# Kernel tuning notes

Measured on AMD Instinct MI355X. Metric: run time of the kernel, lower is better.

The kernel has to match this reference:

```python
import jax, jax.numpy as jnp
import numpy as np

E = 1024  # embed_dim
H = 16    # num_heads
D = E // H  # head_dim
B, S = 2, 2048

def _xavier(key, shape):
    fan_in, fan_out = shape[1], shape[0]
    limit = float(np.sqrt(6.0 / (fan_in + fan_out)))
    return jax.random.uniform(key, shape, jnp.float32, -limit, limit)

def setup_inputs() -> dict:
    key = jax.random.key(0)
    ks = jax.random.split(key, 7)
    return {
        "query": jax.random.normal(ks[0], (B, S, E), jnp.float32),
        "key": jax.random.normal(ks[1], (B, S, E), jnp.float32),
        "value": jax.random.normal(ks[2], (B, S, E), jnp.float32),
        "Wq": _xavier(ks[3], (E, E)), "bq": jnp.zeros((E,), jnp.float32),
        "Wk": _xavier(ks[4], (E, E)), "bk": jnp.zeros((E,), jnp.float32),
        "Wv": _xavier(ks[5], (E, E)), "bv": jnp.zeros((E,), jnp.float32),
        "Wo": _xavier(ks[6], (E, E)), "bo": jnp.zeros((E,), jnp.float32),
    }

def reference(query, key, value, Wq, bq, Wk, bk, Wv, bv, Wo, bo):
    b, s, e = query.shape
    # nn.Linear: x @ W^T + b
    Q = (query @ Wq.T + bq).reshape(b, s, H, D).transpose(0, 2, 1, 3)  # [b,h,s,d]
    K = (key @ Wk.T + bk).reshape(b, s, H, D).transpose(0, 2, 1, 3)
    V = (value @ Wv.T + bv).reshape(b, s, H, D).transpose(0, 2, 1, 3)
    scale = D ** -0.5
    scores = jnp.einsum('bhqd,bhkd->bhqk', Q, K) * scale  # [b,h,s,s]
    attn = jax.nn.softmax(scores, axis=-1)  # dropout=0.0 -> identity
    out = jnp.einsum('bhqk,bhkd->bhqd', attn, V)
    out = out.transpose(0, 2, 1, 3).reshape(b, s, e)
    return out @ Wo.T + bo
```

## Files before the change

kernel.cpp:

```cpp
#include <hip/hip_runtime.h>
#include <stdint.h>

#define E_DIM 1024
#define N_HEADS 16
#define HEAD_D 64
#define BATCH 2
#define SEQ 2048
#define M_ROWS (BATCH*SEQ)

typedef __attribute__((ext_vector_type(8))) short short8;
typedef __attribute__((ext_vector_type(4))) short short4_t;
typedef __attribute__((ext_vector_type(4))) float f32x4;
typedef __attribute__((ext_vector_type(4))) int i32x4;
typedef __attribute__((ext_vector_type(2))) int i32x2;

__device__ __forceinline__ unsigned short f2bf(float f) {
  uint32_t u = __float_as_uint(f);
  u += 0x7FFFu + ((u >> 16) & 1u);
  return (unsigned short)(u >> 16);
}

__device__ __forceinline__ void gload_lds16(const void* g, void* l) {
  __builtin_amdgcn_global_load_lds(
      (const __attribute__((address_space(1))) uint32_t*)(uintptr_t)g,
      (__attribute__((address_space(3))) uint32_t*)(uint32_t)(uintptr_t)l,
      16, 0, 0);
}

__device__ __forceinline__ int cvtpk(float lo, float hi) {
  int r;
  asm("v_cvt_pk_bf16_f32 %0, %1, %2" : "=v"(r) : "v"(lo), "v"(hi));
  return r;
}

__device__ __forceinline__ void cvt_body(const float* __restrict__ src,
                                         unsigned short* __restrict__ dst, int i) {
  f32x4 a = ((const f32x4*)src)[2*i];
  f32x4 b = ((const f32x4*)src)[2*i + 1];
  union { unsigned short us[8]; i32x4 v; } o;
  o.us[0] = f2bf(a[0]); o.us[1] = f2bf(a[1]);
  o.us[2] = f2bf(a[2]); o.us[3] = f2bf(a[3]);
  o.us[4] = f2bf(b[0]); o.us[5] = f2bf(b[1]);
  o.us[6] = f2bf(b[2]); o.us[7] = f2bf(b[3]);
  ((i32x4*)dst)[i] = o.v;
}

__global__ void cvt_all(const float* __restrict__ x0, const float* __restrict__ x1,
                        const float* __restrict__ x2,
                        const float* __restrict__ w0, const float* __restrict__ w1,
                        const float* __restrict__ w2, const float* __restrict__ w3,
                        unsigned short* __restrict__ dx0, unsigned short* __restrict__ dx1,
                        unsigned short* __restrict__ dx2,
                        unsigned short* __restrict__ dw0, unsigned short* __restrict__ dw1,
                        unsigned short* __restrict__ dw2, unsigned short* __restrict__ dw3) {
  const int i = blockIdx.x * blockDim.x + threadIdx.x;
  constexpr int NX8 = M_ROWS * E_DIM / 8;
  constexpr int NW8 = E_DIM * E_DIM / 8;
  if (i < 3 * NX8) {
    const int r = i >> 19, off = i & (NX8 - 1);
    const float* s = (r == 0) ? x0 : (r == 1) ? x1 : x2;
    unsigned short* d = (r == 0) ? dx0 : (r == 1) ? dx1 : dx2;
    cvt_body(s, d, off);
  } else {
    const int j = i - 3 * NX8;
    const int r = j >> 17, off = j & (NW8 - 1);
    const float* s = (r == 0) ? w0 : (r == 1) ? w1 : (r == 2) ? w2 : w3;
    unsigned short* d = (r == 0) ? dw0 : (r == 1) ? dw1 : (r == 2) ? dw2 : dw3;
    cvt_body(s, d, off);
  }
}

__device__ __forceinline__ void gemm_body_rt8(const unsigned short* __restrict__ A,
                                              const unsigned short* __restrict__ Bm,
                                              const float* __restrict__ bias,
                                              unsigned short* __restrict__ Cout,
                                              float scale, int bx, int by,
                                              int Nstr, bool brow) {
  constexpr int BM = 128, BN = 128, BK = 64, K = E_DIM;
  __shared__ __attribute__((aligned(16))) unsigned short Al[2][BM*BK];
  __shared__ __attribute__((aligned(16))) unsigned short Bl[2][BN*BK];
  const int tid  = threadIdx.x;
  const int lane = tid & 63, w = tid >> 6;
  const int wm = w >> 2, wn = w & 3;
  const int l15 = lane & 15, l4 = lane >> 4, l7 = lane & 7;
  const int m0 = by * BM, n0 = bx * BN;
  const int jr = lane >> 3, jc = lane & 7;
  const int kcg = jc ^ jr;

#define GSTAGE(KT, BUF)                                                        \
  do {                                                                         \
    _Pragma("unroll")                                                          \
    for (int t = 0; t < 2; ++t) {                                              \
      int ia = w*2 + t;                                                        \
      const char* src = (const char*)A +                                       \
          ((size_t)(m0 + ia*8 + jr)*K + (KT))*2 + (kcg << 4);                  \
      gload_lds16(src, (char*)Al[BUF] + ia*1024);                              \
    }                                                                          \
    _Pragma("unroll")                                                          \
    for (int t = 0; t < 2; ++t) {                                              \
      int ib = w*2 + t;                                                        \
      const char* src = (const char*)Bm +                                      \
          ((size_t)(n0 + ib*8 + jr)*K + (KT))*2 + (kcg << 4);                  \
      gload_lds16(src, (char*)Bl[BUF] + ib*1024);                              \
    }                                                                          \
  } while (0)

  f32x4 zero = {0.f, 0.f, 0.f, 0.f};
  f32x4 acc[4][2];
  for (int i = 0; i < 4; ++i) for (int j = 0; j < 2; ++j) acc[i][j] = zero;

  GSTAGE(0, 0);
  __syncthreads();

  int cur = 0;
  const int NKT = K / BK;
  for (int kt = 0; kt < NKT; ++kt) {
    if (kt + 1 < NKT) GSTAGE((kt + 1) * BK, cur ^ 1);

#pragma unroll
    for (int ks = 0; ks < 2; ++ks) {
      const int sw = ((ks*4 + l4) ^ l7) << 4;
      short8 af[4], bf[2];
#pragma unroll
      for (int mf = 0; mf < 4; ++mf)
        af[mf] = *(const short8*)((const char*)Al[cur] + (wm*64 + mf*16 + l15)*128 + sw);
#pragma unroll
      for (int nf = 0; nf < 2; ++nf)
        bf[nf] = *(const short8*)((const char*)Bl[cur] + (wn*32 + nf*16 + l15)*128 + sw);
      __builtin_amdgcn_s_setprio(1);
#pragma unroll
      for (int mf = 0; mf < 4; ++mf)
#pragma unroll
        for (int nf = 0; nf < 2; ++nf)
          acc[mf][nf] = __builtin_amdgcn_mfma_f32_16x16x32_bf16(
              af[mf], bf[nf], acc[mf][nf], 0, 0, 0);
      __builtin_amdgcn_s_setprio(0);
    }

    __syncthreads();
    cur ^= 1;
  }
#undef GSTAGE

#pragma unroll
  for (int nf = 0; nf < 2; ++nf) {
    const int col = n0 + wn*32 + nf*16 + l15;
    const float bcol = brow ? 0.f : bias[col];
#pragma unroll
    for (int mf = 0; mf < 4; ++mf) {
      const int rowb = m0 + wm*64 + mf*16 + l4*4;
#pragma unroll
      for (int r = 0; r < 4; ++r) {
        const float bv = brow ? bias[rowb + r] : bcol;
        float v = (acc[mf][nf][r] + bv) * scale;
        Cout[(size_t)(rowb + r)*Nstr + col] = f2bf(v);
      }
    }
  }
}

__global__ __launch_bounds__(512, 4)
void gemm_qkv(const unsigned short* __restrict__ Xq, const unsigned short* __restrict__ Xk,
              const unsigned short* __restrict__ Xv,
              const unsigned short* __restrict__ Wq, const unsigned short* __restrict__ Wk,
              const unsigned short* __restrict__ Wv,
              const float* __restrict__ bq, const float* __restrict__ bk,
              const float* __restrict__ bv,
              unsigned short* __restrict__ Qb, unsigned short* __restrict__ Kb,
              unsigned short* __restrict__ Vt, float scale0) {
  const int z = blockIdx.z;
  const int idx = blockIdx.x;
  if (z == 2) {
    gemm_body_rt8(Wv, Xv, bv, Vt, 1.0f, idx & 31, idx >> 5, M_ROWS, true);
  } else {
    const unsigned short* A  = (z == 0) ? Xq : Xk;
    const unsigned short* Bm = (z == 0) ? Wq : Wk;
    const float* bias        = (z == 0) ? bq : bk;
    unsigned short* C        = (z == 0) ? Qb : Kb;
    const float scale        = (z == 0) ? scale0 : 1.0f;
    gemm_body_rt8(A, Bm, bias, C, scale, idx & 7, idx >> 3, E_DIM, false);
  }
}

__global__ __launch_bounds__(256, 2)
void gemm_o(const unsigned short* __restrict__ A, const unsigned short* __restrict__ Bm,
            const float* __restrict__ bias, float* __restrict__ Cout) {
  constexpr int BM = 128, BN = 64, BK = 64, K = E_DIM, N = E_DIM;
  __shared__ __attribute__((aligned(16))) unsigned short Al[2][BM*BK];
  __shared__ __attribute__((aligned(16))) unsigned short Bl[2][BN*BK];
  const int tid  = threadIdx.x;
  const int lane = tid & 63, w = tid >> 6;
  const int wm = w >> 1, wn = w & 1;
  const int l15 = lane & 15, l4 = lane >> 4, l7 = lane & 7;
  const int m0 = blockIdx.y * BM, n0 = blockIdx.x * BN;
  const int jr = lane >> 3, jc = lane & 7;
  const int kcg = jc ^ jr;

#define GSTAGE(KT, BUF)                                                        \
  do {                                                                         \
    _Pragma("unroll")                                                          \
    for (int t = 0; t < 4; ++t) {                                              \
      int ia = w*4 + t;                                                        \
      const char* src = (const char*)A +                                       \
          ((size_t)(m0 + ia*8 + jr)*K + (KT))*2 + (kcg << 4);                  \
      gload_lds16(src, (char*)Al[BUF] + ia*1024);                              \
    }                                                                          \
    _Pragma("unroll")                                                          \
    for (int t = 0; t < 2; ++t) {                                              \
      int ib = w*2 + t;                                                        \
      const char* src = (const char*)Bm +                                      \
          ((size_t)(n0 + ib*8 + jr)*K + (KT))*2 + (kcg << 4);                  \
      gload_lds16(src, (char*)Bl[BUF] + ib*1024);                              \
    }                                                                          \
  } while (0)

  f32x4 zero = {0.f, 0.f, 0.f, 0.f};
  f32x4 acc[4][2];
  for (int i = 0; i < 4; ++i) for (int j = 0; j < 2; ++j) acc[i][j] = zero;

  GSTAGE(0, 0);
  __syncthreads();

  int cur = 0;
  const int NKT = K / BK;
  for (int kt = 0; kt < NKT; ++kt) {
    if (kt + 1 < NKT) GSTAGE((kt + 1) * BK, cur ^ 1);
#pragma unroll
    for (int ks = 0; ks < 2; ++ks) {
      const int sw = ((ks*4 + l4) ^ l7) << 4;
      short8 af[4], bf[2];
#pragma unroll
      for (int mf = 0; mf < 4; ++mf)
        af[mf] = *(const short8*)((const char*)Al[cur] + (wm*64 + mf*16 + l15)*128 + sw);
#pragma unroll
      for (int nf = 0; nf < 2; ++nf)
        bf[nf] = *(const short8*)((const char*)Bl[cur] + (wn*32 + nf*16 + l15)*128 + sw);
      __builtin_amdgcn_s_setprio(1);
#pragma unroll
      for (int mf = 0; mf < 4; ++mf)
#pragma unroll
        for (int nf = 0; nf < 2; ++nf)
          acc[mf][nf] = __builtin_amdgcn_mfma_f32_16x16x32_bf16(
              af[mf], bf[nf], acc[mf][nf], 0, 0, 0);
      __builtin_amdgcn_s_setprio(0);
    }
    __syncthreads();
    cur ^= 1;
  }
#undef GSTAGE

#pragma unroll
  for (int nf = 0; nf < 2; ++nf) {
    const int col = n0 + wn*32 + nf*16 + l15;
    const float bv = bias[col];
#pragma unroll
    for (int mf = 0; mf < 4; ++mf) {
      const int rowb = m0 + wm*64 + mf*16 + l4*4;
#pragma unroll
      for (int r = 0; r < 4; ++r)
        Cout[(size_t)(rowb + r)*N + col] = acc[mf][nf][r] + bv;
    }
  }
}

__global__ __launch_bounds__(512, 2)
void attn_fwd7(const unsigned short* __restrict__ Q,
               const unsigned short* __restrict__ Kg,
               const unsigned short* __restrict__ Vt_g,
               unsigned short* __restrict__ O) {
  __shared__ __attribute__((aligned(16))) unsigned short Kl[2][4096];
  __shared__ __attribute__((aligned(16))) unsigned short Vl[2][4096];
  __shared__ __attribute__((aligned(16))) unsigned short Pl[8][2][1024];

  const int tid = threadIdx.x;
  const int l = tid & 63, w = tid >> 6;
  const int l15 = l & 15, l4 = l >> 4, l7 = l & 7;

  const int id = blockIdx.x;
  const int bh = (id & 7) * 4 + ((id >> 3) & 3);
  const int qt = id >> 5;
  const int b = bh >> 4, h = bh & 15;
  const size_t bS = (size_t)b * SEQ;
  const int qw = qt * 256 + w * 32;

  short8 qf[2][2];
#pragma unroll
  for (int g = 0; g < 2; ++g) {
    const char* qp = (const char*)Q + ((bS + qw + g*16 + l15) * E_DIM + h * 64) * 2;
    qf[g][0] = *(const short8*)(qp + l4 * 16);
    qf[g][1] = *(const short8*)(qp + 64 + l4 * 16);
  }

  f32x4 zero = {0.f, 0.f, 0.f, 0.f};
  f32x4 oacc[2][4];
#pragma unroll
  for (int g = 0; g < 2; ++g)
#pragma unroll
    for (int i = 0; i < 4; ++i) oacc[g][i] = zero;
  float mrow[2] = {-1e30f, -1e30f}, lrow[2] = {0.f, 0.f};

  const int krow = l >> 3;
  const int kcg  = (l & 7) ^ krow;
  const char* vt_base = (const char*)Vt_g +
      ((size_t)(h * 64 + 8 * w + krow) * M_ROWS + bS) * 2 + (kcg << 4);

#define KSTAGE(KT, BUF)                                                        \
  gload_lds16((const char*)Kg +                                                \
                  ((bS + (size_t)(KT)*64 + 8*w + krow) * E_DIM + h*64 + kcg*8)*2, \
              (char*)Kl[BUF] + w * 1024)

#define VSTAGE(KT, BUF)                                                        \
  gload_lds16(vt_base + (size_t)(KT) * 128, (char*)Vl[BUF] + w * 1024)

  KSTAGE(0, 0);
  VSTAGE(0, 0);
  __syncthreads();

  int cur = 0;
  constexpr int NT = SEQ / 64;
  for (int kt = 0; kt < NT; ++kt) {
    const bool more = (kt + 1 < NT);
    if (more) {
      KSTAGE(kt + 1, cur ^ 1);
      VSTAGE(kt + 1, cur ^ 1);
    }

    short8 kf[8];
    {
      const char* kb = (const char*)Kl[cur];
#pragma unroll
      for (int nf = 0; nf < 4; ++nf) {
        const char* rowb = kb + (nf * 16 + l15) * 128;
        kf[nf*2]     = *(const short8*)(rowb + ((l4 ^ l7) << 4));
        kf[nf*2 + 1] = *(const short8*)(rowb + (((4 + l4) ^ l7) << 4));
      }
    }

    short8 pf[2][2];
#pragma unroll
    for (int g = 0; g < 2; ++g) {
      f32x4 s[4];
      __builtin_amdgcn_s_setprio(1);
#pragma unroll
      for (int nf = 0; nf < 4; ++nf) {
        f32x4 z = zero;
        z = __builtin_amdgcn_mfma_f32_16x16x32_bf16(kf[nf*2],     qf[g][0], z, 0, 0, 0);
        z = __builtin_amdgcn_mfma_f32_16x16x32_bf16(kf[nf*2 + 1], qf[g][1], z, 0, 0, 0);
        s[nf] = z;
      }
      __builtin_amdgcn_s_setprio(0);

      float mx = s[0][0];
#pragma unroll
      for (int nf = 0; nf < 4; ++nf)
#pragma unroll
        for (int r = 0; r < 4; ++r) mx = fmaxf(mx, s[nf][r]);
      mx = fmaxf(mx, __shfl_xor(mx, 16));
      mx = fmaxf(mx, __shfl_xor(mx, 32));
      const float mnew = fmaxf(mrow[g], mx);
      const float fac = __builtin_amdgcn_exp2f(mrow[g] - mnew);
      mrow[g] = mnew;

      float pv[4][4];
      float rs = 0.f;
#pragma unroll
      for (int nf = 0; nf < 4; ++nf)
#pragma unroll
        for (int r = 0; r < 4; ++r) {
          float p = __builtin_amdgcn_exp2f(s[nf][r] - mnew);
          pv[nf][r] = p;
          rs += p;
        }
      rs += __shfl_xor(rs, 16);
      rs += __shfl_xor(rs, 32);
      lrow[g] = lrow[g] * fac + rs;

#pragma unroll
      for (int df = 0; df < 4; ++df)
#pragma unroll
        for (int r = 0; r < 4; ++r) oacc[g][df][r] *= fac;

      char* pw = (char*)&Pl[w][g][0];
#pragma unroll
      for (int nf = 0; nf < 4; ++nf) {
        const int c = nf * 2 + (l4 >> 1);
        i32x2 pk;
        pk.x = cvtpk(pv[nf][0], pv[nf][1]);
        pk.y = cvtpk(pv[nf][2], pv[nf][3]);
        *(i32x2*)(pw + l15 * 128 + ((c ^ l7) << 4) + ((l4 & 1) << 3)) = pk;
      }
      pf[g][0] = *(const short8*)(pw + l15 * 128 + ((l4 ^ l7) << 4));
      pf[g][1] = *(const short8*)(pw + l15 * 128 + (((4 + l4) ^ l7) << 4));
    }

    {
      const char* vbuf = (const char*)Vl[cur];
      __builtin_amdgcn_s_setprio(1);
#pragma unroll
      for (int df = 0; df < 4; ++df) {
        const char* rowb = vbuf + (df * 16 + l15) * 128;
        short8 v0 = *(const short8*)(rowb + ((l4 ^ l7) << 4));
        short8 v1 = *(const short8*)(rowb + (((4 + l4) ^ l7) << 4));
#pragma unroll
        for (int g = 0; g < 2; ++g) {
          oacc[g][df] = __builtin_amdgcn_mfma_f32_16x16x32_bf16(v0, pf[g][0], oacc[g][df], 0, 0, 0);
          oacc[g][df] = __builtin_amdgcn_mfma_f32_16x16x32_bf16(v1, pf[g][1], oacc[g][df], 0, 0, 0);
        }
      }
      __builtin_amdgcn_s_setprio(0);
    }

    __syncthreads();
    cur ^= 1;
  }
#undef KSTAGE
#undef VSTAGE

#pragma unroll
  for (int g = 0; g < 2; ++g) {
    const float rinv = __builtin_amdgcn_rcpf(lrow[g]);
    unsigned short* orow = O + (bS + qw + g*16 + l15) * E_DIM + h * 64;
#pragma unroll
    for (int df = 0; df < 4; ++df) {
      short4_t o4;
#pragma unroll
      for (int r = 0; r < 4; ++r) o4[r] = (short)f2bf(oacc[g][df][r] * rinv);
      *(short4_t*)(orow + df * 16 + l4 * 4) = o4;
    }
  }
}

extern "C" void kernel_launch(void* const* d_in, const int* in_sizes, int n_in,
                              void* d_out, int out_size, void* d_ws, size_t ws_size,
                              hipStream_t stream) {
  const float* q_in = (const float*)d_in[0];
  const float* k_in = (const float*)d_in[1];
  const float* v_in = (const float*)d_in[2];
  const float* Wq = (const float*)d_in[3];
  const float* bq = (const float*)d_in[4];
  const float* Wk = (const float*)d_in[5];
  const float* bk = (const float*)d_in[6];
  const float* Wv = (const float*)d_in[7];
  const float* bv = (const float*)d_in[8];
  const float* Wo = (const float*)d_in[9];
  const float* bo = (const float*)d_in[10];

  char* ws = (char*)d_ws;
  const size_t XB = (size_t)M_ROWS * E_DIM * 2;
  const size_t WB = (size_t)E_DIM * E_DIM * 2;
  unsigned short* Xq  = (unsigned short*)(ws);
  unsigned short* Xk  = (unsigned short*)(ws + XB);
  unsigned short* Xv  = (unsigned short*)(ws + 2*XB);
  unsigned short* Wqb = (unsigned short*)(ws + 3*XB);
  unsigned short* Wkb = (unsigned short*)(ws + 3*XB + WB);
  unsigned short* Wvb = (unsigned short*)(ws + 3*XB + 2*WB);
  unsigned short* Wob = (unsigned short*)(ws + 3*XB + 3*WB);
  unsigned short* Qb  = (unsigned short*)(ws + 3*XB + 4*WB);
  unsigned short* Kb  = (unsigned short*)(ws + 4*XB + 4*WB);
  unsigned short* Vtg = (unsigned short*)(ws + 5*XB + 4*WB);
  unsigned short* Ob  = (unsigned short*)(ws + 6*XB + 4*WB);

  cvt_all<<<8192, 256, 0, stream>>>(q_in, k_in, v_in, Wq, Wk, Wv, Wo,
                                    Xq, Xk, Xv, Wqb, Wkb, Wvb, Wob);

  const float qscale = 0.125f * 1.44269504088896340736f;
  gemm_qkv<<<dim3(256, 1, 3), 512, 0, stream>>>(Xq, Xk, Xv, Wqb, Wkb, Wvb,
                                                bq, bk, bv, Qb, Kb, Vtg, qscale);

  attn_fwd7<<<256, 512, 0, stream>>>(Qb, Kb, Vtg, Ob);

  dim3 ogrid(E_DIM/64, M_ROWS/128);
  gemm_o<<<ogrid, 256, 0, stream>>>(Ob, Wob, bo, (float*)d_out);
}
```

Baseline: 121.9 us.

## Process two K/V tiles per barrier with four-deep LDS buffering in attention

The attention kernel grows its K/V shared-memory ring from 2 to 4 buffers and prefetches the next two 64-key tiles while it computes the current pair. This halves the number of __syncthreads barriers across the key loop and gives the global-to-LDS loads more time to land. In exchange LDS use rises from about 64KB to about 96KB per block. That may limit residency at 2 blocks per CU, and the inlined lambda adds code size and register pressure.

New measurement: 121.0 us, median of 2. No clear change (-0.7%).

```diff
diff --git a/kernel.cpp b/kernel.cpp
--- a/kernel.cpp
+++ b/kernel.cpp
@@ -264,12 +264,12 @@
 }
 
 __global__ __launch_bounds__(512, 2)
-void attn_fwd7(const unsigned short* __restrict__ Q,
+void attn_fwd8(const unsigned short* __restrict__ Q,
                const unsigned short* __restrict__ Kg,
                const unsigned short* __restrict__ Vt_g,
                unsigned short* __restrict__ O) {
-  __shared__ __attribute__((aligned(16))) unsigned short Kl[2][4096];
-  __shared__ __attribute__((aligned(16))) unsigned short Vl[2][4096];
+  __shared__ __attribute__((aligned(16))) unsigned short Kl[4][4096];
+  __shared__ __attribute__((aligned(16))) unsigned short Vl[4][4096];
   __shared__ __attribute__((aligned(16))) unsigned short Pl[8][2][1024];
 
   const int tid = threadIdx.x;
@@ -312,22 +312,10 @@
 #define VSTAGE(KT, BUF)                                                        \
   gload_lds16(vt_base + (size_t)(KT) * 128, (char*)Vl[BUF] + w * 1024)
 
-  KSTAGE(0, 0);
-  VSTAGE(0, 0);
-  __syncthreads();
-
-  int cur = 0;
-  constexpr int NT = SEQ / 64;
-  for (int kt = 0; kt < NT; ++kt) {
-    const bool more = (kt + 1 < NT);
-    if (more) {
-      KSTAGE(kt + 1, cur ^ 1);
-      VSTAGE(kt + 1, cur ^ 1);
-    }
-
+  auto tile_step = [&](int buf) {
     short8 kf[8];
     {
-      const char* kb = (const char*)Kl[cur];
+      const char* kb = (const char*)Kl[buf];
 #pragma unroll
       for (int nf = 0; nf < 4; ++nf) {
         const char* rowb = kb + (nf * 16 + l15) * 128;
@@ -394,7 +382,7 @@
     }
 
     {
-      const char* vbuf = (const char*)Vl[cur];
+      const char* vbuf = (const char*)Vl[buf];
       __builtin_amdgcn_s_setprio(1);
 #pragma unroll
       for (int df = 0; df < 4; ++df) {
@@ -409,9 +397,22 @@
       }
       __builtin_amdgcn_s_setprio(0);
     }
-
+  };
+
+  KSTAGE(0, 0); VSTAGE(0, 0);
+  KSTAGE(1, 1); VSTAGE(1, 1);
+  __syncthreads();
+
+  constexpr int NP = SEQ / 128;
+  for (int p = 0; p < NP; ++p) {
+    const int t0 = 2 * p;
+    if (p + 1 < NP) {
+      KSTAGE(t0 + 2, (t0 + 2) & 3); VSTAGE(t0 + 2, (t0 + 2) & 3);
+      KSTAGE(t0 + 3, (t0 + 3) & 3); VSTAGE(t0 + 3, (t0 + 3) & 3);
+    }
+    tile_step(t0 & 3);
+    tile_step((t0 + 1) & 3);
     __syncthreads();
-    cur ^= 1;
   }
 #undef KSTAGE
 #undef VSTAGE
@@ -467,7 +468,7 @@
   gemm_qkv<<<dim3(256, 1, 3), 512, 0, stream>>>(Xq, Xk, Xv, Wqb, Wkb, Wvb,
                                                 bq, bk, bv, Qb, Kb, Vtg, qscale);
 
-  attn_fwd7<<<256, 512, 0, stream>>>(Qb, Kb, Vtg, Ob);
+  attn_fwd8<<<256, 512, 0, stream>>>(Qb, Kb, Vtg, Ob);
 
   dim3 ogrid(E_DIM/64, M_ROWS/128);
   gemm_o<<<ogrid, 256, 0, stream>>>(Ob, Wob, bo, (float*)d_out);
```
